# Kernel tuning notes

Hardware: AMD Instinct MI355X
Metric: run time of the kernel (lower is better)

The kernel has to match this reference:

```python
import jax, jax.numpy as jnp
import numpy as np

N = 100000      # nodes
E = 3200000     # edges (avg degree 32)
NIN = 16        # node_input_channels
ECH = 16        # edge_channels
F = 10          # node_feature_channels
OUT = 32        # output_channels
ITERS = 3


def _lin(k, fan_in, fan_out):
    kw, kb = jax.random.split(k)
    s = 1.0 / np.sqrt(fan_in)
    W = jax.random.uniform(kw, (fan_in, fan_out), jnp.float32, -s, s)
    b = jax.random.uniform(kb, (fan_out,), jnp.float32, -s, s)
    return W, b


def setup_inputs() -> dict:
    key = jax.random.key(0)
    ks = jax.random.split(key, 11)
    x = jax.random.normal(ks[0], (N, NIN), jnp.float32)
    edge_index = jax.random.randint(ks[1], (2, E), 0, N, jnp.int64)
    edge_attr = jax.random.normal(ks[2], (E, ECH), jnp.float32)
    W1, b1 = _lin(ks[3], NIN, F)
    W2, b2 = _lin(ks[4], F, F)
    W3, b3 = _lin(ks[5], F, F)
    W4, b4 = _lin(ks[6], ECH, F)
    W5, b5 = _lin(ks[7], 2 * F, OUT)
    W6, b6 = _lin(ks[8], F, F)
    W7, b7 = _lin(ks[9], F, F)
    return dict(x=x, edge_index=edge_index, edge_attr=edge_attr,
                W1=W1, b1=b1, W2=W2, b2=b2, W3=W3, b3=b3, W4=W4, b4=b4,
                W5=W5, b5=b5, W6=W6, b6=b6, W7=W7, b7=b7)


def reference(x, edge_index, edge_attr, W1, b1, W2, b2, W3, b3, W4, b4, W5, b5, W6, b6, W7, b7):
    src = edge_index[0]
    dst = edge_index[1]
    n = x.shape[0]

    # loop-invariant pieces (same math, hoisted)
    o1 = x @ W1 + b1                                   # lin1(x), [N, F]
    e = jax.nn.relu(edge_attr @ W4 + b4)               # relu(lin4(edge_attr)), [E, F]
    o3 = jax.ops.segment_sum(e, dst, num_segments=n) @ W3 + b3  # lin3(scatter_add)

    features = jnp.zeros((n, F), x.dtype)
    for _ in range(ITERS):
        # scatter_add over edges with self-loops == segment_sum + identity
        agg = jax.ops.segment_sum(features[src], dst, num_segments=n) + features
        o2 = agg @ W2 + b2
        features = jax.nn.relu(o1 + o2 + o3)

    g = features.sum(axis=0) @ W6 + b6                 # lin6(sum), [F]
    h1 = jnp.broadcast_to(g, (n, F))                   # repeat over nodes
    h2 = features @ W7 + b7                            # lin7(features)
    out = jax.nn.relu(jnp.concatenate([h1, h2], axis=1)) @ W5 + b5
    return out
```

## Files before the change

kernel.cpp:

```cpp
#include <hip/hip_runtime.h>

#define NN 100000
#define NE 3200000
#define NIN 16
#define ECH 16
#define F 10
#define FP 16
#define OC 32
#define CSB 104
#define BKSH 7
#define NBK 782
#define CH 8192

__global__ __launch_bounds__(256) void k_binhist(const int* __restrict__ dst,
                                                 int* __restrict__ bkcnt)
{
    __shared__ int lcnt[NBK];
    int t = threadIdx.x;
    for (int k = t; k < NBK; k += 256) lcnt[k] = 0;
    __syncthreads();
    for (int e = blockIdx.x * 256 + t; e < NE; e += gridDim.x * 256)
        atomicAdd(&lcnt[dst[e] >> BKSH], 1);
    __syncthreads();
    for (int k = t; k < NBK; k += 256) {
        int v = lcnt[k];
        if (v) atomicAdd(&bkcnt[k], v);
    }
}

__global__ __launch_bounds__(1024) void k_bkscan(const int* __restrict__ bkcnt,
                                                 int* __restrict__ bkbase,
                                                 int* __restrict__ offs)
{
    __shared__ int wsum[16], wscan[16];
    int t = threadIdx.x;
    int v = (t < NBK) ? bkcnt[t] : 0;
    int lane = t & 63, w = t >> 6;
    int inc = v;
    for (int d = 1; d < 64; d <<= 1) { int u = __shfl_up(inc, d); if (lane >= d) inc += u; }
    if (lane == 63) wsum[w] = inc;
    __syncthreads();
    if (t < 16) {
        int u = wsum[t];
        for (int d = 1; d < 16; d <<= 1) { int x2 = __shfl_up(u, d); if (t >= d) u += x2; }
        wscan[t] = u;
    }
    __syncthreads();
    int excl = inc - v + (w > 0 ? wscan[w - 1] : 0);
    if (t < NBK) bkbase[t] = excl;
    if (t == 0) { bkbase[NBK] = NE; offs[NN] = NE; }
}

__global__ __launch_bounds__(256) void k_binscat(
    const int* __restrict__ src, const int* __restrict__ dst,
    const int* __restrict__ bkbase, int* __restrict__ cur,
    int* __restrict__ tmp_src, int* __restrict__ tmp_pe)
{
    __shared__ int lcnt[NBK];
    __shared__ int lbb[NBK];
    int t = threadIdx.x;
    int e0 = blockIdx.x * CH;
    int e1 = e0 + CH; if (e1 > NE) e1 = NE;
    for (int k = t; k < NBK; k += 256) lcnt[k] = 0;
    __syncthreads();
    for (int e = e0 + t; e < e1; e += 256)
        atomicAdd(&lcnt[dst[e] >> BKSH], 1);
    __syncthreads();
    for (int k = t; k < NBK; k += 256) {
        int c = lcnt[k];
        lbb[k] = c ? (bkbase[k] + atomicAdd(&cur[k], c)) : 0;
        lcnt[k] = 0;
    }
    __syncthreads();
    for (int e = e0 + t; e < e1; e += 256) {
        int d = dst[e];
        int bk = d >> BKSH;
        int idx = atomicAdd(&lcnt[bk], 1);
        int pos = lbb[bk] + idx;
        tmp_src[pos] = src[e];
        tmp_pe[pos] = ((d & 127) << 22) | e;
    }
}

__global__ __launch_bounds__(256) void k_lsort(
    const int* __restrict__ bkbase,
    const int* __restrict__ tmp_src, const int* __restrict__ tmp_pe,
    int* __restrict__ offs, int* __restrict__ srcs, int* __restrict__ eids)
{
    __shared__ int lcnt[128];
    __shared__ int lcur[128];
    __shared__ int s0tot;
    int t = threadIdx.x;
    int b = blockIdx.x;
    int base = bkbase[b];
    int cnt = bkbase[b + 1] - base;
    int n0 = b << BKSH;
    int nodes = NN - n0; if (nodes > 128) nodes = 128;

    if (t < 128) lcnt[t] = 0;
    __syncthreads();
    for (int i = t; i < cnt; i += 256)
        atomicAdd(&lcnt[tmp_pe[base + i] >> 22], 1);
    __syncthreads();
    if (t < 128) {
        int v = lcnt[t];
        int lane = t & 63, w = t >> 6;
        int inc = v;
        for (int d = 1; d < 64; d <<= 1) { int u = __shfl_up(inc, d); if (lane >= d) inc += u; }
        if (w == 0 && lane == 63) s0tot = inc;
        __syncthreads();
        int excl = inc - v + (w == 1 ? s0tot : 0);
        lcur[t] = base + excl;
        if (t < nodes) offs[n0 + t] = base + excl;
    } else {
        __syncthreads();
    }
    __syncthreads();
    for (int i = t; i < cnt; i += 256) {
        int p = tmp_pe[base + i];
        int d = p >> 22;
        int pos = atomicAdd(&lcur[d], 1);
        srcs[pos] = tmp_src[base + i];
        eids[pos] = p & 0x3FFFFF;
    }
}

__global__ __launch_bounds__(256) void k_init(
    const float* __restrict__ x, const float* __restrict__ ea,
    const int* __restrict__ eids, const int* __restrict__ offs,
    const float* __restrict__ W1, const float* __restrict__ b1,
    const float* __restrict__ b2,
    const float* __restrict__ W3, const float* __restrict__ b3,
    const float* __restrict__ W4, const float* __restrict__ b4,
    float* __restrict__ base, float* __restrict__ feat)
{
    __shared__ float w1[NIN*F], w3[F*F], w4[ECH*F], bb[F], b4s[F];
    int t = threadIdx.x;
    if (t < NIN*F) w1[t] = W1[t];
    if (t < F*F)   w3[t] = W3[t];
    if (t < ECH*F) w4[t] = W4[t];
    if (t < F) { bb[t] = b1[t] + b2[t] + b3[t]; b4s[t] = b4[t]; }
    __syncthreads();

    int wid = t >> 6, l = t & 63;
    int n = blockIdx.x * 4 + wid;
    bool valid = n < NN;
    int p0 = 0, p1 = 0;
    if (valid) { p0 = offs[n]; p1 = offs[n + 1]; }
    int g = l >> 2, sub = l & 3;

    float acc[F];
#pragma unroll
    for (int j = 0; j < F; ++j) acc[j] = 0.f;

    for (int p = p0 + g; p < p1; p += 16) {
        int eid = eids[p];
        float4 av = ((const float4*)(ea + (size_t)eid * ECH))[sub];
        float ev[F];
        int ib = sub * 4;
#pragma unroll
        for (int j = 0; j < F; ++j) {
            float s0 = fmaf(av.x, w4[(ib+0)*F + j], 0.f);
            s0 = fmaf(av.y, w4[(ib+1)*F + j], s0);
            s0 = fmaf(av.z, w4[(ib+2)*F + j], s0);
            s0 = fmaf(av.w, w4[(ib+3)*F + j], s0);
            ev[j] = s0;
        }
#pragma unroll
        for (int j = 0; j < F; ++j) ev[j] += __shfl_xor(ev[j], 1);
#pragma unroll
        for (int j = 0; j < F; ++j) ev[j] += __shfl_xor(ev[j], 2);
#pragma unroll
        for (int j = 0; j < F; ++j) acc[j] += fmaxf(ev[j] + b4s[j], 0.f);
    }
#pragma unroll
    for (int m = 4; m < 64; m <<= 1) {
#pragma unroll
        for (int j = 0; j < F; ++j) acc[j] += __shfl_xor(acc[j], m);
    }

    if (valid) {
        int j = l;
        if (j < F) {
            float a = bb[j];
#pragma unroll
            for (int i = 0; i < NIN; ++i)
                a = fmaf(x[(size_t)n * NIN + i], w1[i*F + j], a);
#pragma unroll
            for (int i = 0; i < F; ++i)
                a = fmaf(acc[i], w3[i*F + j], a);
            base[(size_t)n * FP + j] = a;
            feat[(size_t)n * FP + j] = fmaxf(a, 0.f);
        } else if (j < FP) {
            base[(size_t)n * FP + j] = 0.f;
            feat[(size_t)n * FP + j] = 0.f;
        }
    }
}

__global__ __launch_bounds__(256) void k_iter(
    const int* __restrict__ srcs, const int* __restrict__ offs,
    const float* __restrict__ featO, const float* __restrict__ base,
    const float* __restrict__ W2, float* __restrict__ featN)
{
    __shared__ float w2[F*F];
    __shared__ float sm[4][16];
    int t = threadIdx.x;
    if (t < F*F) w2[t] = W2[t];
    __syncthreads();

    int wid = t >> 6, l = t & 63;
    int n = blockIdx.x * 4 + wid;
    bool valid = n < NN;
    int p0 = 0, p1 = 0;
    if (valid) { p0 = offs[n]; p1 = offs[n + 1]; }
    int g = l >> 2, sub = l & 3;

    float4 a4 = make_float4(0.f, 0.f, 0.f, 0.f);
    for (int p = p0 + g; p < p1; p += 16) {
        int s = srcs[p];
        float4 v = ((const float4*)(featO + (size_t)s * FP))[sub];
        a4.x += v.x; a4.y += v.y; a4.z += v.z; a4.w += v.w;
    }
#pragma unroll
    for (int m = 4; m < 64; m <<= 1) {
        a4.x += __shfl_xor(a4.x, m); a4.y += __shfl_xor(a4.y, m);
        a4.z += __shfl_xor(a4.z, m); a4.w += __shfl_xor(a4.w, m);
    }
    if (valid && l < 4) {
        float4 sv = ((const float4*)(featO + (size_t)n * FP))[l];
        sm[wid][l*4+0] = a4.x + sv.x; sm[wid][l*4+1] = a4.y + sv.y;
        sm[wid][l*4+2] = a4.z + sv.z; sm[wid][l*4+3] = a4.w + sv.w;
    }
    __syncthreads();
    if (valid) {
        int j = l;
        if (j < F) {
            float a = base[(size_t)n * FP + j];
#pragma unroll
            for (int i = 0; i < F; ++i)
                a = fmaf(sm[wid][i], w2[i*F + j], a);
            featN[(size_t)n * FP + j] = fmaxf(a, 0.f);
        } else if (j < FP) {
            featN[(size_t)n * FP + j] = 0.f;
        }
    }
}

__global__ __launch_bounds__(256) void k_colsum(
    const float* __restrict__ feat, float* __restrict__ partial)
{
    __shared__ float sm[4][F];
    int t = threadIdx.x;
    float v[F];
#pragma unroll
    for (int j = 0; j < F; ++j) v[j] = 0.f;
    for (int n = blockIdx.x * 256 + t; n < NN; n += CSB * 256) {
        const float4* p = (const float4*)(feat + (size_t)n * FP);
        float4 v0 = p[0], v1 = p[1], v2 = p[2];
        v[0]+=v0.x; v[1]+=v0.y; v[2]+=v0.z; v[3]+=v0.w;
        v[4]+=v1.x; v[5]+=v1.y; v[6]+=v1.z; v[7]+=v1.w;
        v[8]+=v2.x; v[9]+=v2.y;
    }
#pragma unroll
    for (int off = 32; off > 0; off >>= 1) {
#pragma unroll
        for (int j = 0; j < F; ++j) v[j] += __shfl_down(v[j], off);
    }
    int wid = t >> 6;
    if ((t & 63) == 0) {
#pragma unroll
        for (int j = 0; j < F; ++j) sm[wid][j] = v[j];
    }
    __syncthreads();
    if (t < F) {
        float s = sm[0][t] + sm[1][t] + sm[2][t] + sm[3][t];
        partial[blockIdx.x * F + t] = s;
    }
}

__global__ void k_gsmall(
    const float* __restrict__ partial, const float* __restrict__ W6,
    const float* __restrict__ b6, const float* __restrict__ W5,
    const float* __restrict__ b5, float* __restrict__ gpart)
{
    __shared__ float gcol[F], r1[F];
    int t = threadIdx.x;
    if (t < F) {
        float s = 0.f;
        for (int b = 0; b < CSB; ++b) s += partial[b * F + t];
        gcol[t] = s;
    }
    __syncthreads();
    if (t < F) {
        float acc = b6[t];
        for (int i = 0; i < F; ++i) acc = fmaf(gcol[i], W6[i*F + t], acc);
        r1[t] = acc > 0.f ? acc : 0.f;
    }
    __syncthreads();
    if (t < OC) {
        float acc = b5[t];
        for (int i = 0; i < F; ++i) acc = fmaf(r1[i], W5[i*OC + t], acc);
        gpart[t] = acc;
    }
}

__global__ __launch_bounds__(256) void k_out(
    const float* __restrict__ feat, const float* __restrict__ W7,
    const float* __restrict__ b7, const float* __restrict__ W5,
    const float* __restrict__ gpart, float* __restrict__ out)
{
    __shared__ float w7[F*F], bb7[F], w5[F*OC], gp[OC];
    int t = threadIdx.x;
    if (t < F*F) w7[t] = W7[t];
    if (t < F) bb7[t] = b7[t];
    for (int i = t; i < F*OC; i += 256) w5[i] = W5[F*OC + i];
    if (t < OC) gp[t] = gpart[t];
    __syncthreads();
    int n = blockIdx.x * 256 + t;
    if (n >= NN) return;
    const float4* p = (const float4*)(feat + (size_t)n * FP);
    float4 v0 = p[0], v1 = p[1], v2 = p[2];
    float f[F] = {v0.x,v0.y,v0.z,v0.w, v1.x,v1.y,v1.z,v1.w, v2.x,v2.y};
    float h[F];
#pragma unroll
    for (int j = 0; j < F; ++j) h[j] = bb7[j];
#pragma unroll
    for (int i = 0; i < F; ++i) {
        float fi = f[i];
#pragma unroll
        for (int j = 0; j < F; ++j) h[j] = fmaf(fi, w7[i*F + j], h[j]);
    }
#pragma unroll
    for (int j = 0; j < F; ++j) h[j] = h[j] > 0.f ? h[j] : 0.f;
    float o[OC];
#pragma unroll
    for (int k = 0; k < OC; ++k) o[k] = gp[k];
#pragma unroll
    for (int j = 0; j < F; ++j) {
        float hj = h[j];
#pragma unroll
        for (int k = 0; k < OC; ++k) o[k] = fmaf(hj, w5[j*OC + k], o[k]);
    }
    float4* po = (float4*)(out + (size_t)n * OC);
#pragma unroll
    for (int k = 0; k < 8; ++k)
        po[k] = make_float4(o[4*k], o[4*k+1], o[4*k+2], o[4*k+3]);
}

extern "C" void kernel_launch(void* const* d_in, const int* in_sizes, int n_in,
                              void* d_out, int out_size, void* d_ws, size_t ws_size,
                              hipStream_t stream)
{
    const float* x   = (const float*)d_in[0];
    const int*   ei  = (const int*)d_in[1];
    const float* ea  = (const float*)d_in[2];
    const float* W1  = (const float*)d_in[3];
    const float* b1  = (const float*)d_in[4];
    const float* W2  = (const float*)d_in[5];
    const float* b2  = (const float*)d_in[6];
    const float* W3  = (const float*)d_in[7];
    const float* b3  = (const float*)d_in[8];
    const float* W4  = (const float*)d_in[9];
    const float* b4  = (const float*)d_in[10];
    const float* W5  = (const float*)d_in[11];
    const float* b5  = (const float*)d_in[12];
    const float* W6  = (const float*)d_in[13];
    const float* b6  = (const float*)d_in[14];
    const float* W7  = (const float*)d_in[15];
    const float* b7  = (const float*)d_in[16];

    const int* src = ei;
    const int* dst = ei + NE;

    char* w = (char*)d_ws;
    int* tmp_src = (int*)w;                    w += (size_t)NE * 4;
    int* tmp_pe  = (int*)w;                    w += (size_t)NE * 4;
    int* srcs    = (int*)w;                    w += (size_t)NE * 4;
    int* eids    = (int*)w;                    w += (size_t)NE * 4;
    float* base  = (float*)w;                  w += (size_t)NN * FP * 4;
    float* featA = (float*)w;                  w += (size_t)NN * FP * 4;
    float* featB = (float*)w;                  w += (size_t)NN * FP * 4;
    int* offs    = (int*)w;                    w += (size_t)(NN + 16) * 4;
    int* bkcnt   = (int*)w;                    w += (size_t)NBK * 4;
    int* cur     = (int*)w;                    w += (size_t)NBK * 4;
    int* bkbase  = (int*)w;                    w += (size_t)(NBK + 16) * 4;
    float* partial = (float*)w;                w += (size_t)CSB * F * 4;
    float* gpart = (float*)w;                  w += 32 * 4;

    const int NB = (NN + 255) / 256;
    const int WB = (NN + 3) / 4;
    const int SB = (NE + CH - 1) / CH;

    hipMemsetAsync(bkcnt, 0, (size_t)2 * NBK * 4, stream);

    k_binhist<<<512, 256, 0, stream>>>(dst, bkcnt);
    k_bkscan <<<1, 1024, 0, stream>>>(bkcnt, bkbase, offs);
    k_binscat<<<SB, 256, 0, stream>>>(src, dst, bkbase, cur, tmp_src, tmp_pe);
    k_lsort  <<<NBK, 256, 0, stream>>>(bkbase, tmp_src, tmp_pe, offs, srcs, eids);

    k_init   <<<WB, 256, 0, stream>>>(x, ea, eids, offs, W1, b1, b2, W3, b3,
                                      W4, b4, base, featA);

    k_iter   <<<WB, 256, 0, stream>>>(srcs, offs, featA, base, W2, featB);
    k_iter   <<<WB, 256, 0, stream>>>(srcs, offs, featB, base, W2, featA);

    k_colsum <<<CSB, 256, 0, stream>>>(featA, partial);
    k_gsmall <<<1, 64, 0, stream>>>(partial, W6, b6, W5, b5, gpart);
    k_out    <<<NB, 256, 0, stream>>>(featA, W7, b7, W5, gpart, (float*)d_out);
}
```

Before: 502.4 us.

## Project edges during binning, drop per-node sort, aggregate buckets with LDS atomics

The edge projection relu(lin4(edge_attr)) now runs in the binning pass, reading edge_attr in its original order instead of gathering it through sorted edge ids, and its result is stored as packed bf16. The second-level per-node sort and the CSR offsets are removed. Each 128-node bucket is aggregated by one block using shared-memory float atomics, for both the edge-feature sum and the two propagation iterations. This trades a sort pass and a random gather for many LDS atomics and bf16 rounding of the edge messages, which changes accuracy and makes the summation order nondeterministic.

```diff
diff --git a/kernel.cpp b/kernel.cpp
--- a/kernel.cpp
+++ b/kernel.cpp
@@ -12,6 +12,14 @@
 #define NBK 782
 #define CH 8192
 
+__device__ __forceinline__ unsigned pk_bf16(float a, float b) {
+    unsigned ua = __float_as_uint(a); ua = (ua + 0x7FFFu + ((ua >> 16) & 1u)) >> 16;
+    unsigned ub = __float_as_uint(b); ub = (ub + 0x7FFFu + ((ub >> 16) & 1u)) >> 16;
+    return ua | (ub << 16);
+}
+__device__ __forceinline__ float bf_lo(unsigned u) { return __uint_as_float(u << 16); }
+__device__ __forceinline__ float bf_hi(unsigned u) { return __uint_as_float(u & 0xFFFF0000u); }
+
 __global__ __launch_bounds__(256) void k_binhist(const int* __restrict__ dst,
                                                  int* __restrict__ bkcnt)
 {
@@ -29,8 +37,7 @@
 }
 
 __global__ __launch_bounds__(1024) void k_bkscan(const int* __restrict__ bkcnt,
-                                                 int* __restrict__ bkbase,
-                                                 int* __restrict__ offs)
+                                                 int* __restrict__ bkbase)
 {
     __shared__ int wsum[16], wscan[16];
     int t = threadIdx.x;
@@ -48,17 +55,23 @@
     __syncthreads();
     int excl = inc - v + (w > 0 ? wscan[w - 1] : 0);
     if (t < NBK) bkbase[t] = excl;
-    if (t == 0) { bkbase[NBK] = NE; offs[NN] = NE; }
-}
-
-__global__ __launch_bounds__(256) void k_binscat(
+    if (t == 0) bkbase[NBK] = NE;
+}
+
+__global__ __launch_bounds__(256) void k_binproj(
     const int* __restrict__ src, const int* __restrict__ dst,
+    const float* __restrict__ ea,
     const int* __restrict__ bkbase, int* __restrict__ cur,
-    int* __restrict__ tmp_src, int* __restrict__ tmp_pe)
+    const float* __restrict__ W4, const float* __restrict__ b4,
+    uint4* __restrict__ tmp_e0, unsigned* __restrict__ tmp_e1,
+    unsigned* __restrict__ tmp_sd)
 {
     __shared__ int lcnt[NBK];
     __shared__ int lbb[NBK];
-    int t = threadIdx.x;
+    __shared__ float w4[ECH*F], b4s[F];
+    int t = threadIdx.x;
+    if (t < ECH*F) w4[t] = W4[t];
+    if (t < F) b4s[t] = b4[t];
     int e0 = blockIdx.x * CH;
     int e1 = e0 + CH; if (e1 > NE) e1 = NE;
     for (int k = t; k < NBK; k += 256) lcnt[k] = 0;
@@ -75,175 +88,143 @@
     for (int e = e0 + t; e < e1; e += 256) {
         int d = dst[e];
         int bk = d >> BKSH;
+        const float4* q = (const float4*)(ea + (size_t)e * ECH);
+        float4 a0 = q[0], a1 = q[1], a2 = q[2], a3 = q[3];
+        float av[ECH] = {a0.x,a0.y,a0.z,a0.w, a1.x,a1.y,a1.z,a1.w,
+                         a2.x,a2.y,a2.z,a2.w, a3.x,a3.y,a3.z,a3.w};
+        float ev[F];
+#pragma unroll
+        for (int j = 0; j < F; ++j) ev[j] = b4s[j];
+#pragma unroll
+        for (int i = 0; i < ECH; ++i) {
+            float ai = av[i];
+#pragma unroll
+            for (int j = 0; j < F; ++j) ev[j] = fmaf(ai, w4[i*F + j], ev[j]);
+        }
+#pragma unroll
+        for (int j = 0; j < F; ++j) ev[j] = fmaxf(ev[j], 0.f);
         int idx = atomicAdd(&lcnt[bk], 1);
         int pos = lbb[bk] + idx;
-        tmp_src[pos] = src[e];
-        tmp_pe[pos] = ((d & 127) << 22) | e;
-    }
-}
-
-__global__ __launch_bounds__(256) void k_lsort(
+        tmp_e0[pos] = make_uint4(pk_bf16(ev[0],ev[1]), pk_bf16(ev[2],ev[3]),
+                                 pk_bf16(ev[4],ev[5]), pk_bf16(ev[6],ev[7]));
+        tmp_e1[pos] = pk_bf16(ev[8], ev[9]);
+        tmp_sd[pos] = (unsigned)src[e] | ((unsigned)(d & 127) << 17);
+    }
+}
+
+__global__ __launch_bounds__(256) void k_agg(
+    const float* __restrict__ x,
+    const uint4* __restrict__ tmp_e0, const unsigned* __restrict__ tmp_e1,
+    const unsigned* __restrict__ tmp_sd,
     const int* __restrict__ bkbase,
-    const int* __restrict__ tmp_src, const int* __restrict__ tmp_pe,
-    int* __restrict__ offs, int* __restrict__ srcs, int* __restrict__ eids)
-{
-    __shared__ int lcnt[128];
-    __shared__ int lcur[128];
-    __shared__ int s0tot;
-    int t = threadIdx.x;
-    int b = blockIdx.x;
-    int base = bkbase[b];
-    int cnt = bkbase[b + 1] - base;
-    int n0 = b << BKSH;
-    int nodes = NN - n0; if (nodes > 128) nodes = 128;
-
-    if (t < 128) lcnt[t] = 0;
-    __syncthreads();
-    for (int i = t; i < cnt; i += 256)
-        atomicAdd(&lcnt[tmp_pe[base + i] >> 22], 1);
-    __syncthreads();
-    if (t < 128) {
-        int v = lcnt[t];
-        int lane = t & 63, w = t >> 6;
-        int inc = v;
-        for (int d = 1; d < 64; d <<= 1) { int u = __shfl_up(inc, d); if (lane >= d) inc += u; }
-        if (w == 0 && lane == 63) s0tot = inc;
-        __syncthreads();
-        int excl = inc - v + (w == 1 ? s0tot : 0);
-        lcur[t] = base + excl;
-        if (t < nodes) offs[n0 + t] = base + excl;
-    } else {
-        __syncthreads();
-    }
-    __syncthreads();
-    for (int i = t; i < cnt; i += 256) {
-        int p = tmp_pe[base + i];
-        int d = p >> 22;
-        int pos = atomicAdd(&lcur[d], 1);
-        srcs[pos] = tmp_src[base + i];
-        eids[pos] = p & 0x3FFFFF;
-    }
-}
-
-__global__ __launch_bounds__(256) void k_init(
-    const float* __restrict__ x, const float* __restrict__ ea,
-    const int* __restrict__ eids, const int* __restrict__ offs,
     const float* __restrict__ W1, const float* __restrict__ b1,
     const float* __restrict__ b2,
     const float* __restrict__ W3, const float* __restrict__ b3,
-    const float* __restrict__ W4, const float* __restrict__ b4,
     float* __restrict__ base, float* __restrict__ feat)
 {
-    __shared__ float w1[NIN*F], w3[F*F], w4[ECH*F], bb[F], b4s[F];
+    __shared__ float agg[128][F];
+    __shared__ float w1[NIN*F], w3s[F*F], bb[F];
     int t = threadIdx.x;
     if (t < NIN*F) w1[t] = W1[t];
-    if (t < F*F)   w3[t] = W3[t];
-    if (t < ECH*F) w4[t] = W4[t];
-    if (t < F) { bb[t] = b1[t] + b2[t] + b3[t]; b4s[t] = b4[t]; }
-    __syncthreads();
-
-    int wid = t >> 6, l = t & 63;
-    int n = blockIdx.x * 4 + wid;
-    bool valid = n < NN;
-    int p0 = 0, p1 = 0;
-    if (valid) { p0 = offs[n]; p1 = offs[n + 1]; }
-    int g = l >> 2, sub = l & 3;
-
-    float acc[F];
-#pragma unroll
-    for (int j = 0; j < F; ++j) acc[j] = 0.f;
-
-    for (int p = p0 + g; p < p1; p += 16) {
-        int eid = eids[p];
-        float4 av = ((const float4*)(ea + (size_t)eid * ECH))[sub];
-        float ev[F];
-        int ib = sub * 4;
-#pragma unroll
-        for (int j = 0; j < F; ++j) {
-            float s0 = fmaf(av.x, w4[(ib+0)*F + j], 0.f);
-            s0 = fmaf(av.y, w4[(ib+1)*F + j], s0);
-            s0 = fmaf(av.z, w4[(ib+2)*F + j], s0);
-            s0 = fmaf(av.w, w4[(ib+3)*F + j], s0);
-            ev[j] = s0;
+    if (t < F*F)   w3s[t] = W3[t];
+    if (t < F) bb[t] = b1[t] + b2[t] + b3[t];
+    for (int i = t; i < 128*F; i += 256) ((float*)agg)[i] = 0.f;
+    __syncthreads();
+    int b = blockIdx.x;
+    int bas = bkbase[b], cnt = bkbase[b + 1] - bas;
+    for (int i = t; i < cnt; i += 256) {
+        uint4 h0 = tmp_e0[bas + i];
+        unsigned h1 = tmp_e1[bas + i];
+        unsigned sd = tmp_sd[bas + i];
+        float* row = agg[(sd >> 17) & 127];
+        atomicAdd(row + 0, bf_lo(h0.x)); atomicAdd(row + 1, bf_hi(h0.x));
+        atomicAdd(row + 2, bf_lo(h0.y)); atomicAdd(row + 3, bf_hi(h0.y));
+        atomicAdd(row + 4, bf_lo(h0.z)); atomicAdd(row + 5, bf_hi(h0.z));
+        atomicAdd(row + 6, bf_lo(h0.w)); atomicAdd(row + 7, bf_hi(h0.w));
+        atomicAdd(row + 8, bf_lo(h1));   atomicAdd(row + 9, bf_hi(h1));
+    }
+    __syncthreads();
+    int n0 = b << BKSH;
+    int nodes = NN - n0; if (nodes > 128) nodes = 128;
+    if (t < nodes) {
+        int n = n0 + t;
+        float acc[F];
+#pragma unroll
+        for (int j = 0; j < F; ++j) acc[j] = bb[j];
+#pragma unroll
+        for (int i = 0; i < NIN; ++i) {
+            float xi = x[(size_t)n * NIN + i];
+#pragma unroll
+            for (int j = 0; j < F; ++j) acc[j] = fmaf(xi, w1[i*F + j], acc[j]);
         }
 #pragma unroll
-        for (int j = 0; j < F; ++j) ev[j] += __shfl_xor(ev[j], 1);
-#pragma unroll
-        for (int j = 0; j < F; ++j) ev[j] += __shfl_xor(ev[j], 2);
-#pragma unroll
-        for (int j = 0; j < F; ++j) acc[j] += fmaxf(ev[j] + b4s[j], 0.f);
-    }
-#pragma unroll
-    for (int m = 4; m < 64; m <<= 1) {
-#pragma unroll
-        for (int j = 0; j < F; ++j) acc[j] += __shfl_xor(acc[j], m);
-    }
-
-    if (valid) {
-        int j = l;
-        if (j < F) {
-            float a = bb[j];
-#pragma unroll
-            for (int i = 0; i < NIN; ++i)
-                a = fmaf(x[(size_t)n * NIN + i], w1[i*F + j], a);
-#pragma unroll
-            for (int i = 0; i < F; ++i)
-                a = fmaf(acc[i], w3[i*F + j], a);
-            base[(size_t)n * FP + j] = a;
-            feat[(size_t)n * FP + j] = fmaxf(a, 0.f);
-        } else if (j < FP) {
-            base[(size_t)n * FP + j] = 0.f;
-            feat[(size_t)n * FP + j] = 0.f;
+        for (int i = 0; i < F; ++i) {
+            float ai = agg[t][i];
+#pragma unroll
+            for (int j = 0; j < F; ++j) acc[j] = fmaf(ai, w3s[i*F + j], acc[j]);
         }
-    }
-}
-
-__global__ __launch_bounds__(256) void k_iter(
-    const int* __restrict__ srcs, const int* __restrict__ offs,
+        float4* pb = (float4*)(base + (size_t)n * FP);
+        pb[0] = make_float4(acc[0], acc[1], acc[2], acc[3]);
+        pb[1] = make_float4(acc[4], acc[5], acc[6], acc[7]);
+        pb[2] = make_float4(acc[8], acc[9], 0.f, 0.f);
+        pb[3] = make_float4(0.f, 0.f, 0.f, 0.f);
+        float4* pf = (float4*)(feat + (size_t)n * FP);
+        pf[0] = make_float4(fmaxf(acc[0],0.f), fmaxf(acc[1],0.f), fmaxf(acc[2],0.f), fmaxf(acc[3],0.f));
+        pf[1] = make_float4(fmaxf(acc[4],0.f), fmaxf(acc[5],0.f), fmaxf(acc[6],0.f), fmaxf(acc[7],0.f));
+        pf[2] = make_float4(fmaxf(acc[8],0.f), fmaxf(acc[9],0.f), 0.f, 0.f);
+        pf[3] = make_float4(0.f, 0.f, 0.f, 0.f);
+    }
+}
+
+__global__ __launch_bounds__(256) void k_iterB(
+    const unsigned* __restrict__ tmp_sd, const int* __restrict__ bkbase,
     const float* __restrict__ featO, const float* __restrict__ base,
     const float* __restrict__ W2, float* __restrict__ featN)
 {
+    __shared__ float agg[128][F];
     __shared__ float w2[F*F];
-    __shared__ float sm[4][16];
     int t = threadIdx.x;
     if (t < F*F) w2[t] = W2[t];
-    __syncthreads();
-
-    int wid = t >> 6, l = t & 63;
-    int n = blockIdx.x * 4 + wid;
-    bool valid = n < NN;
-    int p0 = 0, p1 = 0;
-    if (valid) { p0 = offs[n]; p1 = offs[n + 1]; }
-    int g = l >> 2, sub = l & 3;
-
-    float4 a4 = make_float4(0.f, 0.f, 0.f, 0.f);
-    for (int p = p0 + g; p < p1; p += 16) {
-        int s = srcs[p];
-        float4 v = ((const float4*)(featO + (size_t)s * FP))[sub];
-        a4.x += v.x; a4.y += v.y; a4.z += v.z; a4.w += v.w;
-    }
-#pragma unroll
-    for (int m = 4; m < 64; m <<= 1) {
-        a4.x += __shfl_xor(a4.x, m); a4.y += __shfl_xor(a4.y, m);
-        a4.z += __shfl_xor(a4.z, m); a4.w += __shfl_xor(a4.w, m);
-    }
-    if (valid && l < 4) {
-        float4 sv = ((const float4*)(featO + (size_t)n * FP))[l];
-        sm[wid][l*4+0] = a4.x + sv.x; sm[wid][l*4+1] = a4.y + sv.y;
-        sm[wid][l*4+2] = a4.z + sv.z; sm[wid][l*4+3] = a4.w + sv.w;
-    }
-    __syncthreads();
-    if (valid) {
-        int j = l;
-        if (j < F) {
-            float a = base[(size_t)n * FP + j];
-#pragma unroll
-            for (int i = 0; i < F; ++i)
-                a = fmaf(sm[wid][i], w2[i*F + j], a);
-            featN[(size_t)n * FP + j] = fmaxf(a, 0.f);
-        } else if (j < FP) {
-            featN[(size_t)n * FP + j] = 0.f;
+    for (int i = t; i < 128*F; i += 256) ((float*)agg)[i] = 0.f;
+    __syncthreads();
+    int b = blockIdx.x;
+    int bas = bkbase[b], cnt = bkbase[b + 1] - bas;
+    for (int i = t; i < cnt; i += 256) {
+        unsigned sd = tmp_sd[bas + i];
+        int s = sd & 0x1FFFF;
+        const float4* q = (const float4*)(featO + (size_t)s * FP);
+        float4 v0 = q[0], v1 = q[1], v2 = q[2];
+        float* row = agg[(sd >> 17) & 127];
+        atomicAdd(row + 0, v0.x); atomicAdd(row + 1, v0.y);
+        atomicAdd(row + 2, v0.z); atomicAdd(row + 3, v0.w);
+        atomicAdd(row + 4, v1.x); atomicAdd(row + 5, v1.y);
+        atomicAdd(row + 6, v1.z); atomicAdd(row + 7, v1.w);
+        atomicAdd(row + 8, v2.x); atomicAdd(row + 9, v2.y);
+    }
+    __syncthreads();
+    int n0 = b << BKSH;
+    int nodes = NN - n0; if (nodes > 128) nodes = 128;
+    if (t < nodes) {
+        int n = n0 + t;
+        const float4* qs = (const float4*)(featO + (size_t)n * FP);
+        float4 s0 = qs[0], s1 = qs[1], s2 = qs[2];
+        float av[F] = {agg[t][0]+s0.x, agg[t][1]+s0.y, agg[t][2]+s0.z, agg[t][3]+s0.w,
+                       agg[t][4]+s1.x, agg[t][5]+s1.y, agg[t][6]+s1.z, agg[t][7]+s1.w,
+                       agg[t][8]+s2.x, agg[t][9]+s2.y};
+        const float4* pb = (const float4*)(base + (size_t)n * FP);
+        float4 c0 = pb[0], c1 = pb[1], c2 = pb[2];
+        float acc[F] = {c0.x,c0.y,c0.z,c0.w, c1.x,c1.y,c1.z,c1.w, c2.x,c2.y};
+#pragma unroll
+        for (int i = 0; i < F; ++i) {
+            float ai = av[i];
+#pragma unroll
+            for (int j = 0; j < F; ++j) acc[j] = fmaf(ai, w2[i*F + j], acc[j]);
         }
+        float4* pf = (float4*)(featN + (size_t)n * FP);
+        pf[0] = make_float4(fmaxf(acc[0],0.f), fmaxf(acc[1],0.f), fmaxf(acc[2],0.f), fmaxf(acc[3],0.f));
+        pf[1] = make_float4(fmaxf(acc[4],0.f), fmaxf(acc[5],0.f), fmaxf(acc[6],0.f), fmaxf(acc[7],0.f));
+        pf[2] = make_float4(fmaxf(acc[8],0.f), fmaxf(acc[9],0.f), 0.f, 0.f);
+        pf[3] = make_float4(0.f, 0.f, 0.f, 0.f);
     }
 }
 
@@ -374,14 +355,12 @@
     const int* dst = ei + NE;
 
     char* w = (char*)d_ws;
-    int* tmp_src = (int*)w;                    w += (size_t)NE * 4;
-    int* tmp_pe  = (int*)w;                    w += (size_t)NE * 4;
-    int* srcs    = (int*)w;                    w += (size_t)NE * 4;
-    int* eids    = (int*)w;                    w += (size_t)NE * 4;
+    uint4* tmp_e0   = (uint4*)w;               w += (size_t)NE * 16;
+    unsigned* tmp_e1 = (unsigned*)w;           w += (size_t)NE * 4;
+    unsigned* tmp_sd = (unsigned*)w;           w += (size_t)NE * 4;
     float* base  = (float*)w;                  w += (size_t)NN * FP * 4;
     float* featA = (float*)w;                  w += (size_t)NN * FP * 4;
     float* featB = (float*)w;                  w += (size_t)NN * FP * 4;
-    int* offs    = (int*)w;                    w += (size_t)(NN + 16) * 4;
     int* bkcnt   = (int*)w;                    w += (size_t)NBK * 4;
     int* cur     = (int*)w;                    w += (size_t)NBK * 4;
     int* bkbase  = (int*)w;                    w += (size_t)(NBK + 16) * 4;
@@ -389,21 +368,20 @@
     float* gpart = (float*)w;                  w += 32 * 4;
 
     const int NB = (NN + 255) / 256;
-    const int WB = (NN + 3) / 4;
     const int SB = (NE + CH - 1) / CH;
 
     hipMemsetAsync(bkcnt, 0, (size_t)2 * NBK * 4, stream);
 
     k_binhist<<<512, 256, 0, stream>>>(dst, bkcnt);
-    k_bkscan <<<1, 1024, 0, stream>>>(bkcnt, bkbase, offs);
-    k_binscat<<<SB, 256, 0, stream>>>(src, dst, bkbase, cur, tmp_src, tmp_pe);
-    k_lsort  <<<NBK, 256, 0, stream>>>(bkbase, tmp_src, tmp_pe, offs, srcs, eids);
-
-    k_init   <<<WB, 256, 0, stream>>>(x, ea, eids, offs, W1, b1, b2, W3, b3,
-                                      W4, b4, base, featA);
-
-    k_iter   <<<WB, 256, 0, stream>>>(srcs, offs, featA, base, W2, featB);
-    k_iter   <<<WB, 256, 0, stream>>>(srcs, offs, featB, base, W2, featA);
+    k_bkscan <<<1, 1024, 0, stream>>>(bkcnt, bkbase);
+    k_binproj<<<SB, 256, 0, stream>>>(src, dst, ea, bkbase, cur, W4, b4,
+                                      tmp_e0, tmp_e1, tmp_sd);
+
+    k_agg    <<<NBK, 256, 0, stream>>>(x, tmp_e0, tmp_e1, tmp_sd, bkbase,
+                                       W1, b1, b2, W3, b3, base, featA);
+
+    k_iterB  <<<NBK, 256, 0, stream>>>(tmp_sd, bkbase, featA, base, W2, featB);
+    k_iterB  <<<NBK, 256, 0, stream>>>(tmp_sd, bkbase, featB, base, W2, featA);
 
     k_colsum <<<CSB, 256, 0, stream>>>(featA, partial);
     k_gsmall <<<1, 64, 0, stream>>>(partial, W6, b6, W5, b5, gpart);
```

Result: slower. 915.8 us (+82.3%).

## Store iteration features in bf16 and unroll gather loops by two

Applied to the files above, without the earlier changes.

Node features passed between the message-passing iterations are stored as packed bf16 (8 uint words per node) instead of padded fp32, halving the bytes per random gather in k_iter. The edge and feature gather loops in k_init and k_iter are unrolled by two for more outstanding loads. The binning pass also writes src and packed dst/eid as one int2 instead of two separate arrays. bf16 rounding of intermediate features adds numerical error that may approach tolerance limits.

```diff
diff --git a/kernel.cpp b/kernel.cpp
--- a/kernel.cpp
+++ b/kernel.cpp
@@ -12,6 +12,14 @@
 #define NBK 782
 #define CH 8192
 
+__device__ __forceinline__ unsigned pk_bf16(float a, float b) {
+    unsigned ua = __float_as_uint(a); ua = (ua + 0x7FFFu + ((ua >> 16) & 1u)) >> 16;
+    unsigned ub = __float_as_uint(b); ub = (ub + 0x7FFFu + ((ub >> 16) & 1u)) >> 16;
+    return ua | (ub << 16);
+}
+__device__ __forceinline__ float bf_lo(unsigned u) { return __uint_as_float(u << 16); }
+__device__ __forceinline__ float bf_hi(unsigned u) { return __uint_as_float(u & 0xFFFF0000u); }
+
 __global__ __launch_bounds__(256) void k_binhist(const int* __restrict__ dst,
                                                  int* __restrict__ bkcnt)
 {
@@ -54,7 +62,7 @@
 __global__ __launch_bounds__(256) void k_binscat(
     const int* __restrict__ src, const int* __restrict__ dst,
     const int* __restrict__ bkbase, int* __restrict__ cur,
-    int* __restrict__ tmp_src, int* __restrict__ tmp_pe)
+    int2* __restrict__ pair)
 {
     __shared__ int lcnt[NBK];
     __shared__ int lbb[NBK];
@@ -76,15 +84,12 @@
         int d = dst[e];
         int bk = d >> BKSH;
         int idx = atomicAdd(&lcnt[bk], 1);
-        int pos = lbb[bk] + idx;
-        tmp_src[pos] = src[e];
-        tmp_pe[pos] = ((d & 127) << 22) | e;
+        pair[lbb[bk] + idx] = make_int2(src[e], ((d & 127) << 22) | e);
     }
 }
 
 __global__ __launch_bounds__(256) void k_lsort(
-    const int* __restrict__ bkbase,
-    const int* __restrict__ tmp_src, const int* __restrict__ tmp_pe,
+    const int* __restrict__ bkbase, const int2* __restrict__ pair,
     int* __restrict__ offs, int* __restrict__ srcs, int* __restrict__ eids)
 {
     __shared__ int lcnt[128];
@@ -100,7 +105,7 @@
     if (t < 128) lcnt[t] = 0;
     __syncthreads();
     for (int i = t; i < cnt; i += 256)
-        atomicAdd(&lcnt[tmp_pe[base + i] >> 22], 1);
+        atomicAdd(&lcnt[((unsigned)pair[base + i].y) >> 22], 1);
     __syncthreads();
     if (t < 128) {
         int v = lcnt[t];
@@ -117,11 +122,11 @@
     }
     __syncthreads();
     for (int i = t; i < cnt; i += 256) {
-        int p = tmp_pe[base + i];
-        int d = p >> 22;
-        int pos = atomicAdd(&lcur[d], 1);
-        srcs[pos] = tmp_src[base + i];
-        eids[pos] = p & 0x3FFFFF;
+        int2 pr = pair[base + i];
+        int pe = pr.y;
+        int pos = atomicAdd(&lcur[((unsigned)pe) >> 22], 1);
+        srcs[pos] = pr.x;
+        eids[pos] = pe & 0x3FFFFF;
     }
 }
 
@@ -132,7 +137,7 @@
     const float* __restrict__ b2,
     const float* __restrict__ W3, const float* __restrict__ b3,
     const float* __restrict__ W4, const float* __restrict__ b4,
-    float* __restrict__ base, float* __restrict__ feat)
+    float* __restrict__ base, unsigned* __restrict__ fb)
 {
     __shared__ float w1[NIN*F], w3[F*F], w4[ECH*F], bb[F], b4s[F];
     int t = threadIdx.x;
@@ -148,16 +153,43 @@
     int p0 = 0, p1 = 0;
     if (valid) { p0 = offs[n]; p1 = offs[n + 1]; }
     int g = l >> 2, sub = l & 3;
+    int ib = sub * 4;
 
     float acc[F];
 #pragma unroll
     for (int j = 0; j < F; ++j) acc[j] = 0.f;
 
-    for (int p = p0 + g; p < p1; p += 16) {
-        int eid = eids[p];
-        float4 av = ((const float4*)(ea + (size_t)eid * ECH))[sub];
+    int p = p0 + g;
+    for (; p + 16 < p1; p += 32) {
+        int e0 = eids[p], e1 = eids[p + 16];
+        float4 av0 = ((const float4*)(ea + (size_t)e0 * ECH))[sub];
+        float4 av1 = ((const float4*)(ea + (size_t)e1 * ECH))[sub];
+        float ev0[F], ev1[F];
+#pragma unroll
+        for (int j = 0; j < F; ++j) {
+            float s0 = fmaf(av0.x, w4[(ib+0)*F + j], 0.f);
+            s0 = fmaf(av0.y, w4[(ib+1)*F + j], s0);
+            s0 = fmaf(av0.z, w4[(ib+2)*F + j], s0);
+            s0 = fmaf(av0.w, w4[(ib+3)*F + j], s0);
+            ev0[j] = s0;
+            float s1 = fmaf(av1.x, w4[(ib+0)*F + j], 0.f);
+            s1 = fmaf(av1.y, w4[(ib+1)*F + j], s1);
+            s1 = fmaf(av1.z, w4[(ib+2)*F + j], s1);
+            s1 = fmaf(av1.w, w4[(ib+3)*F + j], s1);
+            ev1[j] = s1;
+        }
+#pragma unroll
+        for (int j = 0; j < F; ++j) { ev0[j] += __shfl_xor(ev0[j], 1); ev1[j] += __shfl_xor(ev1[j], 1); }
+#pragma unroll
+        for (int j = 0; j < F; ++j) { ev0[j] += __shfl_xor(ev0[j], 2); ev1[j] += __shfl_xor(ev1[j], 2); }
+#pragma unroll
+        for (int j = 0; j < F; ++j)
+            acc[j] += fmaxf(ev0[j] + b4s[j], 0.f) + fmaxf(ev1[j] + b4s[j], 0.f);
+    }
+    if (p < p1) {
+        int e0 = eids[p];
+        float4 av = ((const float4*)(ea + (size_t)e0 * ECH))[sub];
         float ev[F];
-        int ib = sub * 4;
 #pragma unroll
         for (int j = 0; j < F; ++j) {
             float s0 = fmaf(av.x, w4[(ib+0)*F + j], 0.f);
@@ -179,6 +211,7 @@
         for (int j = 0; j < F; ++j) acc[j] += __shfl_xor(acc[j], m);
     }
 
+    float fv = 0.f;
     if (valid) {
         int j = l;
         if (j < F) {
@@ -190,18 +223,22 @@
             for (int i = 0; i < F; ++i)
                 a = fmaf(acc[i], w3[i*F + j], a);
             base[(size_t)n * FP + j] = a;
-            feat[(size_t)n * FP + j] = fmaxf(a, 0.f);
+            fv = fmaxf(a, 0.f);
         } else if (j < FP) {
             base[(size_t)n * FP + j] = 0.f;
-            feat[(size_t)n * FP + j] = 0.f;
         }
     }
+    float partner = __shfl_xor(fv, 1);
+    if (valid && l < 16 && (l & 1) == 0)
+        fb[(size_t)n * 8 + (l >> 1)] = pk_bf16(fv, partner);
 }
 
 __global__ __launch_bounds__(256) void k_iter(
     const int* __restrict__ srcs, const int* __restrict__ offs,
-    const float* __restrict__ featO, const float* __restrict__ base,
-    const float* __restrict__ W2, float* __restrict__ featN)
+    const uint2* __restrict__ fbO, const float* __restrict__ base,
+    const float* __restrict__ W2,
+    unsigned* __restrict__ fbN, float* __restrict__ featN,
+    int wfb, int wf32)
 {
     __shared__ float w2[F*F];
     __shared__ float sm[4][16];
@@ -217,10 +254,21 @@
     int g = l >> 2, sub = l & 3;
 
     float4 a4 = make_float4(0.f, 0.f, 0.f, 0.f);
-    for (int p = p0 + g; p < p1; p += 16) {
-        int s = srcs[p];
-        float4 v = ((const float4*)(featO + (size_t)s * FP))[sub];
-        a4.x += v.x; a4.y += v.y; a4.z += v.z; a4.w += v.w;
+    int p = p0 + g;
+    for (; p + 16 < p1; p += 32) {
+        int s0 = srcs[p], s1 = srcs[p + 16];
+        uint2 v0 = fbO[(size_t)s0 * 4 + sub];
+        uint2 v1 = fbO[(size_t)s1 * 4 + sub];
+        a4.x += bf_lo(v0.x) + bf_lo(v1.x);
+        a4.y += bf_hi(v0.x) + bf_hi(v1.x);
+        a4.z += bf_lo(v0.y) + bf_lo(v1.y);
+        a4.w += bf_hi(v0.y) + bf_hi(v1.y);
+    }
+    if (p < p1) {
+        int s0 = srcs[p];
+        uint2 v0 = fbO[(size_t)s0 * 4 + sub];
+        a4.x += bf_lo(v0.x); a4.y += bf_hi(v0.x);
+        a4.z += bf_lo(v0.y); a4.w += bf_hi(v0.y);
     }
 #pragma unroll
     for (int m = 4; m < 64; m <<= 1) {
@@ -228,27 +276,32 @@
         a4.z += __shfl_xor(a4.z, m); a4.w += __shfl_xor(a4.w, m);
     }
     if (valid && l < 4) {
-        float4 sv = ((const float4*)(featO + (size_t)n * FP))[l];
-        sm[wid][l*4+0] = a4.x + sv.x; sm[wid][l*4+1] = a4.y + sv.y;
-        sm[wid][l*4+2] = a4.z + sv.z; sm[wid][l*4+3] = a4.w + sv.w;
-    }
-    __syncthreads();
+        uint2 sv = fbO[(size_t)n * 4 + l];
+        sm[wid][l*4+0] = a4.x + bf_lo(sv.x); sm[wid][l*4+1] = a4.y + bf_hi(sv.x);
+        sm[wid][l*4+2] = a4.z + bf_lo(sv.y); sm[wid][l*4+3] = a4.w + bf_hi(sv.y);
+    }
+    __syncthreads();
+    float fv = 0.f;
+    if (valid && l < F) {
+        float a = base[(size_t)n * FP + l];
+#pragma unroll
+        for (int i = 0; i < F; ++i)
+            a = fmaf(sm[wid][i], w2[i*F + l], a);
+        fv = fmaxf(a, 0.f);
+    }
+    float partner = __shfl_xor(fv, 1);
     if (valid) {
-        int j = l;
-        if (j < F) {
-            float a = base[(size_t)n * FP + j];
-#pragma unroll
-            for (int i = 0; i < F; ++i)
-                a = fmaf(sm[wid][i], w2[i*F + j], a);
-            featN[(size_t)n * FP + j] = fmaxf(a, 0.f);
-        } else if (j < FP) {
-            featN[(size_t)n * FP + j] = 0.f;
+        if (wfb && l < 16 && (l & 1) == 0)
+            fbN[(size_t)n * 8 + (l >> 1)] = pk_bf16(fv, partner);
+        if (wf32) {
+            if (l < F) featN[(size_t)n * FP + l] = fv;
+            else if (l < FP) featN[(size_t)n * FP + l] = 0.f;
         }
     }
 }
 
 __global__ __launch_bounds__(256) void k_colsum(
-    const float* __restrict__ feat, float* __restrict__ partial)
+    const float* __restrict__ feat, float* __restrict__ cpart)
 {
     __shared__ float sm[4][F];
     int t = threadIdx.x;
@@ -275,12 +328,12 @@
     __syncthreads();
     if (t < F) {
         float s = sm[0][t] + sm[1][t] + sm[2][t] + sm[3][t];
-        partial[blockIdx.x * F + t] = s;
+        cpart[blockIdx.x * F + t] = s;
     }
 }
 
 __global__ void k_gsmall(
-    const float* __restrict__ partial, const float* __restrict__ W6,
+    const float* __restrict__ cpart, const float* __restrict__ W6,
     const float* __restrict__ b6, const float* __restrict__ W5,
     const float* __restrict__ b5, float* __restrict__ gpart)
 {
@@ -288,7 +341,7 @@
     int t = threadIdx.x;
     if (t < F) {
         float s = 0.f;
-        for (int b = 0; b < CSB; ++b) s += partial[b * F + t];
+        for (int b = 0; b < CSB; ++b) s += cpart[b * F + t];
         gcol[t] = s;
     }
     __syncthreads();
@@ -374,18 +427,18 @@
     const int* dst = ei + NE;
 
     char* w = (char*)d_ws;
-    int* tmp_src = (int*)w;                    w += (size_t)NE * 4;
-    int* tmp_pe  = (int*)w;                    w += (size_t)NE * 4;
+    int2* pair   = (int2*)w;                   w += (size_t)NE * 8;
     int* srcs    = (int*)w;                    w += (size_t)NE * 4;
     int* eids    = (int*)w;                    w += (size_t)NE * 4;
     float* base  = (float*)w;                  w += (size_t)NN * FP * 4;
     float* featA = (float*)w;                  w += (size_t)NN * FP * 4;
-    float* featB = (float*)w;                  w += (size_t)NN * FP * 4;
+    unsigned* fbA = (unsigned*)w;              w += (size_t)NN * 32;
+    unsigned* fbB = (unsigned*)w;              w += (size_t)NN * 32;
     int* offs    = (int*)w;                    w += (size_t)(NN + 16) * 4;
     int* bkcnt   = (int*)w;                    w += (size_t)NBK * 4;
     int* cur     = (int*)w;                    w += (size_t)NBK * 4;
     int* bkbase  = (int*)w;                    w += (size_t)(NBK + 16) * 4;
-    float* partial = (float*)w;                w += (size_t)CSB * F * 4;
+    float* cpart = (float*)w;                  w += (size_t)CSB * F * 4;
     float* gpart = (float*)w;                  w += 32 * 4;
 
     const int NB = (NN + 255) / 256;
@@ -396,16 +449,18 @@
 
     k_binhist<<<512, 256, 0, stream>>>(dst, bkcnt);
     k_bkscan <<<1, 1024, 0, stream>>>(bkcnt, bkbase, offs);
-    k_binscat<<<SB, 256, 0, stream>>>(src, dst, bkbase, cur, tmp_src, tmp_pe);
-    k_lsort  <<<NBK, 256, 0, stream>>>(bkbase, tmp_src, tmp_pe, offs, srcs, eids);
+    k_binscat<<<SB, 256, 0, stream>>>(src, dst, bkbase, cur, pair);
+    k_lsort  <<<NBK, 256, 0, stream>>>(bkbase, pair, offs, srcs, eids);
 
     k_init   <<<WB, 256, 0, stream>>>(x, ea, eids, offs, W1, b1, b2, W3, b3,
-                                      W4, b4, base, featA);
-
-    k_iter   <<<WB, 256, 0, stream>>>(srcs, offs, featA, base, W2, featB);
-    k_iter   <<<WB, 256, 0, stream>>>(srcs, offs, featB, base, W2, featA);
-
-    k_colsum <<<CSB, 256, 0, stream>>>(featA, partial);
-    k_gsmall <<<1, 64, 0, stream>>>(partial, W6, b6, W5, b5, gpart);
+                                      W4, b4, base, fbA);
+
+    k_iter   <<<WB, 256, 0, stream>>>(srcs, offs, (const uint2*)fbA, base, W2,
+                                      fbB, (float*)nullptr, 1, 0);
+    k_iter   <<<WB, 256, 0, stream>>>(srcs, offs, (const uint2*)fbB, base, W2,
+                                      (unsigned*)nullptr, featA, 0, 1);
+
+    k_colsum <<<CSB, 256, 0, stream>>>(featA, cpart);
+    k_gsmall <<<1, 64, 0, stream>>>(cpart, W6, b6, W5, b5, gpart);
     k_out    <<<NB, 256, 0, stream>>>(featA, W7, b7, W5, gpart, (float*)d_out);
 }
```

New measurement: 450.8 us. 10.3% less time.
